# Performance work log

Measured on AMD Instinct MI355X. Metric: run time of the kernel, lower is better.

The kernel has to match this reference:

```python
import jax, jax.numpy as jnp
import numpy as np
import math

B, D_IN, D_MODEL, N_LAYERS, N_HALF, D_OUT = 32, 100, 256, 4, 32, 1
K_ENC = 64               # ConvTranspose2d kernel -> 64x64 feature map from 1x1 latent
L_SEQ = K_ENC * K_ENC    # 4096 flattened spatial sequence for S4D
DT_MIN, DT_MAX = 0.001, 0.1


def setup_inputs() -> dict:
    key = jax.random.key(0)
    ks = jax.random.split(key, 8)
    x = jax.random.normal(ks[0], (B, D_IN, 1, 1), jnp.float32)
    # encoder ConvTranspose2d weight: (in, out, kh, kw)
    enc_w = jax.random.normal(ks[1], (D_IN, D_MODEL, K_ENC, K_ENC), jnp.float32) * 0.02
    # S4D kernel params per layer (stacked over layers)
    log_dt = math.log(DT_MIN) + jax.random.uniform(ks[2], (N_LAYERS, D_MODEL), jnp.float32) * (
        math.log(DT_MAX) - math.log(DT_MIN))
    C = jax.random.normal(ks[3], (N_LAYERS, D_MODEL, N_HALF, 2), jnp.float32)  # complex C as (re, im)
    log_A_real = jnp.log(0.5 * jnp.ones((N_LAYERS, D_MODEL, N_HALF), jnp.float32))
    A_imag = jnp.tile(math.pi * jnp.arange(N_HALF, dtype=jnp.float32), (N_LAYERS, D_MODEL, 1))
    Dskip = jax.random.normal(ks[4], (N_LAYERS, D_MODEL), jnp.float32)
    # output_linear: Conv1d(H, 2H, 1) followed by GLU(dim=-2)
    out_w = jax.random.normal(ks[5], (N_LAYERS, 2 * D_MODEL, D_MODEL), jnp.float32) / math.sqrt(D_MODEL)
    out_b = jnp.zeros((N_LAYERS, 2 * D_MODEL), jnp.float32)
    # decoder: Conv2d(d_model, d_output, 1)
    dec_w = jax.random.normal(ks[6], (D_OUT, D_MODEL), jnp.float32) / math.sqrt(D_MODEL)
    dec_b = jnp.zeros((D_OUT,), jnp.float32)
    return dict(x=x, enc_w=enc_w, log_dt=log_dt, C=C, log_A_real=log_A_real,
                A_imag=A_imag, Dskip=Dskip, out_w=out_w, out_b=out_b,
                dec_w=dec_w, dec_b=dec_b)


def s4d_kernel(log_dt, C, log_A_real, A_imag, L):
    """S4D convolution kernel via Vandermonde: returns (H, L) real kernel."""
    dt = jnp.exp(log_dt)                       # (H,)
    Cc = C[..., 0] + 1j * C[..., 1]            # (H, N)
    A = -jnp.exp(log_A_real) + 1j * A_imag     # (H, N) diagonal state matrix
    dtA = A * dt[:, None]                      # (H, N)
    V = jnp.exp(dtA[:, :, None] * jnp.arange(L, dtype=log_dt.dtype))  # (H, N, L) Vandermonde
    Cc = Cc * (jnp.exp(dtA) - 1.0) / A         # ZOH discretization of C
    return 2.0 * jnp.einsum('hn,hnl->hl', Cc, V).real  # (H, L)


def s4d_layer(u, log_dt, C, log_A_real, A_imag, Dskip, out_w, out_b):
    """u: (B, H, L) -> (B, H, L). FFT convolution + skip + GELU + 1x1 conv + GLU."""
    L = u.shape[-1]
    k = s4d_kernel(log_dt, C, log_A_real, A_imag, L)
    k_f = jnp.fft.rfft(k, n=2 * L)             # (H, L+1)
    u_f = jnp.fft.rfft(u, n=2 * L)             # (B, H, L+1)
    y = jnp.fft.irfft(u_f * k_f, n=2 * L)[..., :L]
    y = y + u * Dskip[:, None]
    y = jax.nn.gelu(y, approximate=False)      # torch nn.GELU (exact erf)
    y = jnp.einsum('oh,bhl->bol', out_w, y) + out_b[:, None]  # Conv1d(H, 2H, 1)
    a, b = jnp.split(y, 2, axis=1)             # GLU along channel dim
    return a * jax.nn.sigmoid(b)


def reference(x, enc_w, log_dt, C, log_A_real, A_imag, Dskip, out_w, out_b, dec_w, dec_b):
    # encoder: ConvTranspose2d(kernel=64, stride=4, bias=False) on a 1x1 input
    # is exactly an outer product of latent with the kernel.
    h = jnp.einsum('bixy,iohw->bohw', x, enc_w)        # (B, D_MODEL, 64, 64)
    Bb, Hc, Hh, Ww = h.shape
    h = h.reshape(Bb, Hc, Hh * Ww)                     # (B, H, L) flattened spatial sequence
    for i in range(N_LAYERS):                          # prenorm=False -> no LayerNorm applied
        z = s4d_layer(h, log_dt[i], C[i], log_A_real[i], A_imag[i],
                      Dskip[i], out_w[i], out_b[i])
        h = z + h                                      # residual
    y = jnp.einsum('oc,bcl->bol', dec_w, h) + dec_b[:, None]  # Conv2d 1x1 decoder
    return y.reshape(Bb, D_OUT, Hh, Ww)
```

## Files before the change

### kernel.cpp

```cpp
#include <hip/hip_runtime.h>
#include <hip/hip_bf16.h>
#include <math.h>

#pragma clang fp contract(off)

#define BB   32
#define DIN  100
#define HH   256
#define NLAY 4
#define NH   32
#define LL   4096
#define LC   128
#define NC   32
#define HL   (HH*LL)
#define BLn  (BB*LL)

typedef __attribute__((ext_vector_type(8))) short s8v;
typedef __attribute__((ext_vector_type(4))) float f4v;

__device__ inline unsigned short f2b(float x) {
    unsigned int u = __float_as_uint(x);
    unsigned int r = (u + 0x7fffu + ((u >> 16) & 1u)) >> 16;
    return (unsigned short)r;
}
__device__ inline float b2f(unsigned short u) {
    return __uint_as_float(((unsigned int)u) << 16);
}

__global__ __launch_bounds__(256) void k_enc(const float* __restrict__ x,
                                             const float* __restrict__ ew,
                                             unsigned short* __restrict__ hb) {
    __shared__ unsigned short xs[BB*128];
    __shared__ unsigned short ot[BB*264];
    int tid = threadIdx.x;
    for (int idx = tid; idx < BB*128; idx += 256) {
        int b = idx >> 7, k = idx & 127;
        float v = (k < DIN) ? x[b*DIN + k] : 0.f;
        int slot = (k >> 3) ^ (b & 7);
        xs[b*128 + slot*8 + (k & 7)] = f2b(v);
    }
    __syncthreads();
    int hl0 = blockIdx.x * 256;
    int h = hl0 >> 12, l0 = hl0 & 4095;
    int w = tid >> 6, l = tid & 63;
    int l16 = l & 15, lk8 = (l >> 4) * 8, e4 = (l >> 4) * 4;
    int col0 = w * 64;
    f4v acc[2][4];
    #pragma unroll
    for (int i = 0; i < 2; i++)
        #pragma unroll
        for (int j = 0; j < 4; j++) acc[i][j] = (f4v){0.f,0.f,0.f,0.f};
    #pragma unroll
    for (int ks = 0; ks < 4; ks++) {
        int kb = ks*32 + lk8;
        int sl0 = kb >> 3;
        s8v a0 = *(const s8v*)&xs[l16*128 + (sl0 ^ (l16 & 7))*8];
        s8v a1 = *(const s8v*)&xs[(16 + l16)*128 + (sl0 ^ (l16 & 7))*8];
        #pragma unroll
        for (int j = 0; j < 4; j++) {
            int hl = hl0 + col0 + j*16 + l16;
            const float* ep = ew + (size_t)kb * HL + hl;
            s8v bf;
            #pragma unroll
            for (int q = 0; q < 8; q++) {
                float ev = (kb + q < DIN) ? ep[(size_t)q * HL] : 0.f;
                bf[q] = (short)f2b(ev);
            }
            acc[0][j] = __builtin_amdgcn_mfma_f32_16x16x32_bf16(a0, bf, acc[0][j], 0, 0, 0);
            acc[1][j] = __builtin_amdgcn_mfma_f32_16x16x32_bf16(a1, bf, acc[1][j], 0, 0, 0);
        }
    }
    #pragma unroll
    for (int i = 0; i < 2; i++)
        #pragma unroll
        for (int j = 0; j < 4; j++) {
            int cl = col0 + j*16 + l16;
            #pragma unroll
            for (int e = 0; e < 4; e++) {
                int b = i*16 + e4 + e;
                ot[b*264 + cl] = f2b(acc[i][j][e]);
            }
        }
    __syncthreads();
    {
        int b = tid >> 3, off = (tid & 7) * 32;
        const unsigned short* src = &ot[b*264 + off];
        unsigned short* dst = &hb[(size_t)h*BLn + (size_t)b*LL + l0 + off];
        #pragma unroll
        for (int q = 0; q < 4; q++)
            *(s8v*)(dst + q*8) = *(const s8v*)(src + q*8);
    }
}

__global__ __launch_bounds__(256) void k_prep1(const float* __restrict__ ldt,
        const float* __restrict__ Cp, const float* __restrict__ lAr,
        const float* __restrict__ Aimp,
        float* __restrict__ pdta, float* __restrict__ pwlc, float* __restrict__ pcd2) {
    int g = blockIdx.x*256 + threadIdx.x;
    int layer = g >> 13, h = (g >> 5) & 255, n = g & 31;
    float dt  = expf(ldt[layer*HH + h]);
    float are = -expf(lAr[(layer*HH + h)*NH + n]);
    float aim = Aimp[(layer*HH + h)*NH + n];
    float dre = are*dt, dimg = aim*dt;
    float er = expf(dre);
    float s, c; sincosf(dimg, &s, &c);
    float wre = er*c, wim = er*s;
    float den = are*are + aim*aim;
    float nre = wre - 1.f, nim = wim;
    float qre = (nre*are + nim*aim)/den;
    float qim = (nim*are - nre*aim)/den;
    float cre = Cp[((layer*HH + h)*NH + n)*2 + 0];
    float cim = Cp[((layer*HH + h)*NH + n)*2 + 1];
    float dcr = cre*qre - cim*qim;
    float dci = cre*qim + cim*qre;
    pcd2[g*2+0] = 2.f*dcr;  pcd2[g*2+1] = 2.f*dci;
    pdta[g*2+0] = dre;      pdta[g*2+1] = dimg;
    float erl = expf(dre*(float)LC);
    float sl, cl; sincosf(dimg*(float)LC, &sl, &cl);
    pwlc[g*2+0] = erl*cl;   pwlc[g*2+1] = erl*sl;
}

__global__ __launch_bounds__(256) void k_bldAll(const float* __restrict__ pdta,
        const float* __restrict__ pcd2, unsigned short* __restrict__ AstB,
        unsigned short* __restrict__ AcvB) {
    __shared__ float dre_s[NH], dim_s[NH], c2r[NH], c2i[NH];
    __shared__ float kkl[LC];
    int bid = blockIdx.x;
    int tid = threadIdx.x;
    int pbase = bid * 64;
    if (tid < NH) {
        dre_s[tid] = pdta[pbase + tid*2];
        dim_s[tid] = pdta[pbase + tid*2 + 1];
        c2r[tid]   = pcd2[pbase + tid*2];
        c2i[tid]   = pcd2[pbase + tid*2 + 1];
    }
    __syncthreads();
    if (tid < LC) {
        float fm = (float)tid;
        float acc = 0.f;
        for (int n = 0; n < NH; n++) {
            float er = expf(dre_s[n]*fm);
            float s, c; sincosf(dim_s[n]*fm, &s, &c);
            acc += c2r[n]*er*c - c2i[n]*er*s;
        }
        kkl[tid] = acc;
    }
    __syncthreads();
    unsigned short* As = AstB + (size_t)bid * 8192;
    for (int idx = tid; idx < 8192; idx += 256) {
        int r = idx >> 7, m = idx & 127, n = r >> 1;
        float e = (float)(127 - m);
        float er = expf(dre_s[n]*e);
        float s, c; sincosf(dim_s[n]*e, &s, &c);
        As[idx] = f2b((r & 1) ? er*s : er*c);
    }
    unsigned short* Ac = AcvB + (size_t)bid * 24576;
    for (int idx = tid; idx < 24576; idx += 256) {
        int j = idx / 192, k = idx - j*192;
        float v;
        if (k < 128) {
            v = (j >= k) ? kkl[j - k] : 0.f;
        } else {
            int n = (k - 128) >> 1;
            float e = (float)(j + 1);
            float er = expf(dre_s[n]*e);
            float s, c; sincosf(dim_s[n]*e, &s, &c);
            v = ((k - 128) & 1) ? (-er*s) : (er*c);
        }
        Ac[idx] = f2b(v);
    }
}

__global__ __launch_bounds__(256) void k_prepW(const float* __restrict__ outw,
                                               unsigned short* __restrict__ Wbf) {
    int t = blockIdx.x*256 + threadIdx.x;
    Wbf[t] = f2b(outw[t]);
}

__global__ __launch_bounds__(256) void k_BG(const unsigned short* __restrict__ AstB,
        const unsigned short* __restrict__ AcvB, const unsigned short* __restrict__ hb,
        const float* __restrict__ pwlc, const float* __restrict__ pcd2,
        const float* __restrict__ DskL, unsigned short* __restrict__ Ybf) {
    __shared__ unsigned short Ul[64*128];
    __shared__ unsigned short Fl[64*64];
    int g = blockIdx.x;
    int h  = (g & 7)*32 + (g >> 7);
    int ct = (g >> 3) & 15;
    int tid = threadIdx.x;
    const unsigned short* ub = hb + (size_t)h*BLn + (size_t)ct*64*LC;
    #pragma unroll
    for (int it = 0; it < 4; it++) {
        int idx = it*256 + tid;
        int col = idx >> 4, slot = idx & 15;
        s8v v = *(const s8v*)(ub + col*LC + slot*8);
        *(s8v*)&Ul[col*128 + (slot ^ (col & 7))*8] = v;
    }
    __syncthreads();
    int w = tid >> 6, l = tid & 63;
    int l16 = l & 15, lk8 = (l >> 4)*8, e4 = (l >> 4)*4, k8q = l >> 4;

    {
        f4v facc[4];
        #pragma unroll
        for (int j = 0; j < 4; j++) facc[j] = (f4v){0.f,0.f,0.f,0.f};
        const unsigned short* Ab = AstB + (size_t)h*8192 + (w*16 + l16)*128;
        #pragma unroll
        for (int ks = 0; ks < 4; ks++) {
            s8v af = *(const s8v*)(Ab + ks*32 + lk8);
            int k8 = ks*4 + k8q;
            #pragma unroll
            for (int j = 0; j < 4; j++) {
                int col = j*16 + l16;
                s8v bf = *(const s8v*)&Ul[col*128 + (k8 ^ (col & 7))*8];
                facc[j] = __builtin_amdgcn_mfma_f32_16x16x32_bf16(af, bf, facc[j], 0, 0, 0);
            }
        }
        #pragma unroll
        for (int j = 0; j < 4; j++) {
            int col = j*16 + l16;
            int idx = (col*64 + w*16 + e4) ^ ((col & 7) << 3);
            *(ushort4*)&Fl[idx] = make_ushort4(f2b(facc[j][0]), f2b(facc[j][1]),
                                               f2b(facc[j][2]), f2b(facc[j][3]));
        }
    }
    __syncthreads();

    if (tid < 64) {
        int n = tid & 31, bl = tid >> 5;
        int hn2 = (h*NH + n)*2;
        float wlr = pwlc[hn2], wli = pwlc[hn2+1];
        float cr  = pcd2[hn2], ci  = pcd2[hn2+1];
        float sr = 0.f, si = 0.f;
        #pragma unroll 4
        for (int c = 0; c < NC; c++) {
            int lcol = bl*32 + c;
            int idx = (lcol*64 + 2*n) ^ ((lcol & 7) << 3);
            ushort2 fv = *(ushort2*)&Fl[idx];
            float fr = b2f(fv.x), fi = b2f(fv.y);
            *(ushort2*)&Fl[idx] = make_ushort2(f2b(cr*sr - ci*si), f2b(cr*si + ci*sr));
            float nsr = fmaf(wlr, sr, fmaf(-wli, si, fr));
            si = fmaf(wlr, si, fmaf(wli, sr, fi));
            sr = nsr;
        }
    }
    __syncthreads();

    float dsk = DskL[h];
    const unsigned short* Cb = AcvB + (size_t)h*24576;
    f4v acc[2][4];
    #pragma unroll
    for (int i = 0; i < 2; i++)
        #pragma unroll
        for (int j = 0; j < 4; j++) acc[i][j] = (f4v){0.f,0.f,0.f,0.f};
    #pragma unroll
    for (int ks = 0; ks < 4; ks++) {
        s8v af0 = *(const s8v*)(Cb + (w*32 + l16)*192 + ks*32 + lk8);
        s8v af1 = *(const s8v*)(Cb + (w*32 + 16 + l16)*192 + ks*32 + lk8);
        int k8 = ks*4 + k8q;
        #pragma unroll
        for (int j = 0; j < 4; j++) {
            int col = j*16 + l16;
            s8v bf = *(const s8v*)&Ul[col*128 + (k8 ^ (col & 7))*8];
            acc[0][j] = __builtin_amdgcn_mfma_f32_16x16x32_bf16(af0, bf, acc[0][j], 0, 0, 0);
            acc[1][j] = __builtin_amdgcn_mfma_f32_16x16x32_bf16(af1, bf, acc[1][j], 0, 0, 0);
        }
    }
    #pragma unroll
    for (int ks = 0; ks < 2; ks++) {
        s8v af0 = *(const s8v*)(Cb + (w*32 + l16)*192 + 128 + ks*32 + lk8);
        s8v af1 = *(const s8v*)(Cb + (w*32 + 16 + l16)*192 + 128 + ks*32 + lk8);
        int kk2 = ks*32 + lk8;
        #pragma unroll
        for (int j = 0; j < 4; j++) {
            int col = j*16 + l16;
            int idx = (col*64 + kk2) ^ ((col & 7) << 3);
            s8v bf = *(const s8v*)&Fl[idx];
            acc[0][j] = __builtin_amdgcn_mfma_f32_16x16x32_bf16(af0, bf, acc[0][j], 0, 0, 0);
            acc[1][j] = __builtin_amdgcn_mfma_f32_16x16x32_bf16(af1, bf, acc[1][j], 0, 0, 0);
        }
    }
    unsigned short* Yb = Ybf + (size_t)h*BLn + (size_t)ct*64*LC;
    #pragma unroll
    for (int i = 0; i < 2; i++) {
        int m0 = w*32 + i*16 + e4;
        int sl = m0 >> 3, off = m0 & 7;
        #pragma unroll
        for (int j = 0; j < 4; j++) {
            int col = j*16 + l16;
            ushort4 u4 = *(const ushort4*)&Ul[col*128 + (sl ^ (col & 7))*8 + off];
            float uu[4] = {b2f(u4.x), b2f(u4.y), b2f(u4.z), b2f(u4.w)};
            unsigned short ov[4];
            #pragma unroll
            for (int e = 0; e < 4; e++) {
                float yv = fmaf(dsk, uu[e], acc[i][j][e]);
                ov[e] = f2b(0.5f*yv*(1.f + erff(yv*0.70710678118f)));
            }
            *(ushort4*)&Yb[col*LC + m0] = make_ushort4(ov[0], ov[1], ov[2], ov[3]);
        }
    }
}

__global__ __launch_bounds__(512) void k_gC2(const unsigned short* __restrict__ Wb,
        const float* __restrict__ outb, const unsigned short* __restrict__ Ybf,
        unsigned short* __restrict__ hb, const float* __restrict__ dw,
        const float* __restrict__ db, float* __restrict__ outp, int doDec) {
    __shared__ __align__(16) unsigned char smem[34048];
    unsigned short* Bl = (unsigned short*)smem;
    float* part = (float*)smem;
    int nt = blockIdx.x;
    int n0 = nt*64;
    int tid = threadIdx.x;

    {
        int jn = (tid & 15) * 4;
        int hq = tid >> 4;
        #pragma unroll
        for (int hb8 = 0; hb8 < 8; hb8++) {
            int h = hb8*32 + hq;
            ushort4 v = *(const ushort4*)&Ybf[(size_t)h*BLn + n0 + jn];
            unsigned short vv[4] = {v.x, v.y, v.z, v.w};
            #pragma unroll
            for (int i = 0; i < 4; i++) {
                int row = jn + i;
                Bl[row*258 + (h ^ ((row & 7) << 3))] = vv[i];
            }
        }
    }
    __syncthreads();

    int w = tid >> 6, l = tid & 63;
    int l16 = l & 15, lk8 = (l >> 4) * 8, e4 = (l >> 4) * 4;
    int ra = w*32 + l16;
    int swz = (l16 & 7) << 3;
    f4v acc[4][4];
    #pragma unroll
    for (int i = 0; i < 4; i++)
        #pragma unroll
        for (int j = 0; j < 4; j++) acc[i][j] = (f4v){0.f,0.f,0.f,0.f};
    const unsigned short* W0 = Wb + ra*HH;
    const unsigned short* W1 = Wb + (ra+16)*HH;
    const unsigned short* W2 = Wb + (ra+256)*HH;
    const unsigned short* W3 = Wb + (ra+272)*HH;
    #pragma unroll
    for (int ks = 0; ks < 8; ks++) {
        int kk = ks*32 + lk8;
        s8v a0 = *(const s8v*)(W0 + kk);
        s8v a1 = *(const s8v*)(W1 + kk);
        s8v a2 = *(const s8v*)(W2 + kk);
        s8v a3 = *(const s8v*)(W3 + kk);
        s8v bfv[4];
        #pragma unroll
        for (int j = 0; j < 4; j++) {
            int row = j*16 + l16;
            bfv[j] = *(const s8v*)&Bl[row*258 + (kk ^ swz)];
        }
        #pragma unroll
        for (int j = 0; j < 4; j++) {
            acc[0][j] = __builtin_amdgcn_mfma_f32_16x16x32_bf16(a0, bfv[j], acc[0][j], 0, 0, 0);
            acc[1][j] = __builtin_amdgcn_mfma_f32_16x16x32_bf16(a1, bfv[j], acc[1][j], 0, 0, 0);
            acc[2][j] = __builtin_amdgcn_mfma_f32_16x16x32_bf16(a2, bfv[j], acc[2][j], 0, 0, 0);
            acc[3][j] = __builtin_amdgcn_mfma_f32_16x16x32_bf16(a3, bfv[j], acc[3][j], 0, 0, 0);
        }
    }

    float pj[4] = {0.f, 0.f, 0.f, 0.f};
    #pragma unroll
    for (int i = 0; i < 2; i++) {
        int ob = w*32 + i*16 + e4;
        #pragma unroll
        for (int e = 0; e < 4; e++) {
            int o = ob + e;
            float ba  = outb[o];
            float bb2 = outb[o + 256];
            float dwo = doDec ? dw[o] : 0.f;
            #pragma unroll
            for (int j = 0; j < 4; j++) {
                float za = acc[i][j][e] + ba;
                float zb = acc[i+2][j][e] + bb2;
                float sig = 1.f/(1.f + expf(-zb));
                unsigned short* hp = &hb[(size_t)o*BLn + n0 + j*16 + l16];
                float hnew = fmaf(za, sig, b2f(*hp));
                if (doDec) {
                    pj[j] = fmaf(dwo, hnew, pj[j]);
                } else {
                    *hp = f2b(hnew);
                }
            }
        }
    }

    if (doDec) {
        __syncthreads();
        int g32 = w*4 + (l >> 4);
        #pragma unroll
        for (int j = 0; j < 4; j++) {
            int nl = j*16 + l16;
            part[nl*33 + g32] = pj[j];
        }
        __syncthreads();
        if (tid < 64) {
            float s = db[0];
            #pragma unroll
            for (int g = 0; g < 32; g++) s += part[tid*33 + g];
            outp[n0 + tid] = s;
        }
    }
}

extern "C" void kernel_launch(void* const* d_in, const int* in_sizes, int n_in,
                              void* d_out, int out_size, void* d_ws, size_t ws_size,
                              hipStream_t stream) {
    (void)in_sizes; (void)n_in; (void)out_size; (void)ws_size;
    const float* x    = (const float*)d_in[0];
    const float* ew   = (const float*)d_in[1];
    const float* ldt  = (const float*)d_in[2];
    const float* Cp   = (const float*)d_in[3];
    const float* lAr  = (const float*)d_in[4];
    const float* Aimp = (const float*)d_in[5];
    const float* Dsk  = (const float*)d_in[6];
    const float* outw = (const float*)d_in[7];
    const float* outb = (const float*)d_in[8];
    const float* dw   = (const float*)d_in[9];
    const float* db   = (const float*)d_in[10];

    float* ws = (float*)d_ws;
    unsigned short* hb  = (unsigned short*)ws;
    unsigned short* Ybf = (unsigned short*)(ws + 16777216UL);
    unsigned short* AstB= (unsigned short*)(ws + 33554432UL);
    unsigned short* AcvB= (unsigned short*)(ws + 37748736UL);
    unsigned short* Wbf = (unsigned short*)(ws + 50331648UL);
    float* pdta = ws + 50593792UL;
    float* pwlc = ws + 50659328UL;
    float* pcd2 = ws + 50724864UL;

    k_prep1<<<128, 256, 0, stream>>>(ldt, Cp, lAr, Aimp, pdta, pwlc, pcd2);
    k_bldAll<<<1024, 256, 0, stream>>>(pdta, pcd2, AstB, AcvB);
    k_prepW<<<2048, 256, 0, stream>>>(outw, Wbf);
    k_enc<<<4096, 256, 0, stream>>>(x, ew, hb);
    for (int layer = 0; layer < NLAY; layer++) {
        k_BG<<<4096, 256, 0, stream>>>(AstB + (size_t)layer*2097152,
                                       AcvB + (size_t)layer*6291456, hb,
                                       pwlc + layer*16384, pcd2 + layer*16384,
                                       Dsk + layer*HH, Ybf);
        k_gC2<<<2048, 512, 0, stream>>>(Wbf + layer*131072, outb + layer*512, Ybf, hb,
                                        dw, db, (float*)d_out, (layer == NLAY-1) ? 1 : 0);
    }
}
```

Before: 990.3 us.

## Fuse per-layer S4D and GLU kernels into a persistent megakernel with flag sync

Replaces the eight per-layer launches of k_BG and k_gC2 with one persistent kernel of 512 blocks. Each block processes several tiles, and the stages are ordered with per-group atomic counters in global memory plus spin waits, so no kernel-boundary barriers are needed. The intent is to cut launch overhead and the tail idle time at each boundary, and to let independent groups move ahead of each other. The risks are a deadlock if not all 512 blocks are co-resident, lower occupancy from the larger shared memory footprint, and spin-wait overhead.

```diff
diff --git a/kernel.cpp b/kernel.cpp
--- a/kernel.cpp
+++ b/kernel.cpp
@@ -29,10 +29,12 @@
 
 __global__ __launch_bounds__(256) void k_enc(const float* __restrict__ x,
                                              const float* __restrict__ ew,
-                                             unsigned short* __restrict__ hb) {
+                                             unsigned short* __restrict__ hb,
+                                             int* __restrict__ flags) {
     __shared__ unsigned short xs[BB*128];
     __shared__ unsigned short ot[BB*264];
     int tid = threadIdx.x;
+    if (blockIdx.x == 0 && tid < 128) flags[tid] = 0;
     for (int idx = tid; idx < BB*128; idx += 256) {
         int b = idx >> 7, k = idx & 127;
         float v = (k < DIN) ? x[b*DIN + k] : 0.f;
@@ -177,16 +179,20 @@
     Wbf[t] = f2b(outw[t]);
 }
 
-__global__ __launch_bounds__(256) void k_BG(const unsigned short* __restrict__ AstB,
-        const unsigned short* __restrict__ AcvB, const unsigned short* __restrict__ hb,
-        const float* __restrict__ pwlc, const float* __restrict__ pcd2,
-        const float* __restrict__ DskL, unsigned short* __restrict__ Ybf) {
-    __shared__ unsigned short Ul[64*128];
-    __shared__ unsigned short Fl[64*64];
-    int g = blockIdx.x;
-    int h  = (g & 7)*32 + (g >> 7);
-    int ct = (g >> 3) & 15;
-    int tid = threadIdx.x;
+__device__ __forceinline__ void waitflag(int* p, int target) {
+    if (threadIdx.x == 0) {
+        while (__hip_atomic_load(p, __ATOMIC_RELAXED, __HIP_MEMORY_SCOPE_AGENT) < target)
+            __builtin_amdgcn_s_sleep(2);
+    }
+    __syncthreads();
+    __threadfence();
+}
+
+__device__ __forceinline__ void bg_tile(unsigned short* Ul, unsigned short* Fl,
+        const unsigned short* AstL, const unsigned short* AcvL,
+        const unsigned short* hb, const float* pwlcL, const float* pcd2L,
+        const float* DskL, unsigned short* Ybf, int h, int ct, int tid) {
+    __syncthreads();
     const unsigned short* ub = hb + (size_t)h*BLn + (size_t)ct*64*LC;
     #pragma unroll
     for (int it = 0; it < 4; it++) {
@@ -203,7 +209,7 @@
         f4v facc[4];
         #pragma unroll
         for (int j = 0; j < 4; j++) facc[j] = (f4v){0.f,0.f,0.f,0.f};
-        const unsigned short* Ab = AstB + (size_t)h*8192 + (w*16 + l16)*128;
+        const unsigned short* Ab = AstL + (size_t)h*8192 + (w*16 + l16)*128;
         #pragma unroll
         for (int ks = 0; ks < 4; ks++) {
             s8v af = *(const s8v*)(Ab + ks*32 + lk8);
@@ -228,8 +234,8 @@
     if (tid < 64) {
         int n = tid & 31, bl = tid >> 5;
         int hn2 = (h*NH + n)*2;
-        float wlr = pwlc[hn2], wli = pwlc[hn2+1];
-        float cr  = pcd2[hn2], ci  = pcd2[hn2+1];
+        float wlr = pwlcL[hn2], wli = pwlcL[hn2+1];
+        float cr  = pcd2L[hn2], ci  = pcd2L[hn2+1];
         float sr = 0.f, si = 0.f;
         #pragma unroll 4
         for (int c = 0; c < NC; c++) {
@@ -246,7 +252,7 @@
     __syncthreads();
 
     float dsk = DskL[h];
-    const unsigned short* Cb = AcvB + (size_t)h*24576;
+    const unsigned short* Cb = AcvL + (size_t)h*24576;
     f4v acc[2][4];
     #pragma unroll
     for (int i = 0; i < 2; i++)
@@ -300,17 +306,14 @@
     }
 }
 
-__global__ __launch_bounds__(512) void k_gC2(const unsigned short* __restrict__ Wb,
-        const float* __restrict__ outb, const unsigned short* __restrict__ Ybf,
-        unsigned short* __restrict__ hb, const float* __restrict__ dw,
-        const float* __restrict__ db, float* __restrict__ outp, int doDec) {
-    __shared__ __align__(16) unsigned char smem[34048];
+__device__ __forceinline__ void gc2_tile(unsigned char* smem,
+        const unsigned short* WbL, const float* outbL,
+        const unsigned short* Ybf, unsigned short* hb, const float* dw,
+        const float* db, float* outp, int nt, int doDec, int tid) {
     unsigned short* Bl = (unsigned short*)smem;
     float* part = (float*)smem;
-    int nt = blockIdx.x;
     int n0 = nt*64;
-    int tid = threadIdx.x;
-
+    __syncthreads();
     {
         int jn = (tid & 15) * 4;
         int hq = tid >> 4;
@@ -337,10 +340,10 @@
     for (int i = 0; i < 4; i++)
         #pragma unroll
         for (int j = 0; j < 4; j++) acc[i][j] = (f4v){0.f,0.f,0.f,0.f};
-    const unsigned short* W0 = Wb + ra*HH;
-    const unsigned short* W1 = Wb + (ra+16)*HH;
-    const unsigned short* W2 = Wb + (ra+256)*HH;
-    const unsigned short* W3 = Wb + (ra+272)*HH;
+    const unsigned short* W0 = WbL + ra*HH;
+    const unsigned short* W1 = WbL + (ra+16)*HH;
+    const unsigned short* W2 = WbL + (ra+256)*HH;
+    const unsigned short* W3 = WbL + (ra+272)*HH;
     #pragma unroll
     for (int ks = 0; ks < 8; ks++) {
         int kk = ks*32 + lk8;
@@ -370,8 +373,8 @@
         #pragma unroll
         for (int e = 0; e < 4; e++) {
             int o = ob + e;
-            float ba  = outb[o];
-            float bb2 = outb[o + 256];
+            float ba  = outbL[o];
+            float bb2 = outbL[o + 256];
             float dwo = doDec ? dw[o] : 0.f;
             #pragma unroll
             for (int j = 0; j < 4; j++) {
@@ -403,6 +406,58 @@
             #pragma unroll
             for (int g = 0; g < 32; g++) s += part[tid*33 + g];
             outp[n0 + tid] = s;
+        }
+    }
+}
+
+__global__ __launch_bounds__(512, 4) void k_mega(
+        const unsigned short* __restrict__ AstB, const unsigned short* __restrict__ AcvB,
+        unsigned short* __restrict__ hb, unsigned short* __restrict__ Ybf,
+        const float* __restrict__ pwlc, const float* __restrict__ pcd2,
+        const float* __restrict__ Dsk, const unsigned short* __restrict__ Wbf,
+        const float* __restrict__ outb, const float* __restrict__ dw,
+        const float* __restrict__ db, float* __restrict__ outp,
+        int* __restrict__ flags) {
+    __shared__ __align__(16) unsigned char smem[49664];
+    int tid = threadIdx.x;
+    int g = blockIdx.x;
+    int s = tid >> 8;
+    int tid256 = tid & 255;
+    int grp = g >> 5;
+    unsigned short* Ul = (unsigned short*)(smem + s*24576);
+    unsigned short* Fl = (unsigned short*)(smem + s*24576 + 16384);
+    int* cnt1 = flags;
+    int* cnt2 = flags + 64;
+
+    for (int L = 0; L < NLAY; L++) {
+        if (L) waitflag(&cnt2[(L-1)*16 + grp], 128);
+        const unsigned short* AstL = AstB + (size_t)L*2097152;
+        const unsigned short* AcvL = AcvB + (size_t)L*6291456;
+        const float* pwlcL = pwlc + L*16384;
+        const float* pcd2L = pcd2 + L*16384;
+        const float* DskL  = Dsk + L*HH;
+        #pragma unroll 1
+        for (int i = 0; i < 4; i++) {
+            int T = g*8 + s*4 + i;
+            bg_tile(Ul, Fl, AstL, AcvL, hb, pwlcL, pcd2L, DskL, Ybf,
+                    T & 255, T >> 8, tid256);
+        }
+        __threadfence();
+        __syncthreads();
+        if (tid == 0) atomicAdd(&cnt1[L*16 + grp], 8);
+        waitflag(&cnt1[L*16 + grp], 256);
+
+        const unsigned short* WbL  = Wbf + L*131072;
+        const float* outbL = outb + L*512;
+        int doDec = (L == NLAY-1) ? 1 : 0;
+        #pragma unroll 1
+        for (int j = 0; j < 4; j++) {
+            gc2_tile(smem, WbL, outbL, Ybf, hb, dw, db, outp, g*4 + j, doDec, tid);
+        }
+        if (L < NLAY-1) {
+            __threadfence();
+            __syncthreads();
+            if (tid == 0) atomicAdd(&cnt2[L*16 + grp], 4);
         }
     }
 }
@@ -432,17 +487,12 @@
     float* pdta = ws + 50593792UL;
     float* pwlc = ws + 50659328UL;
     float* pcd2 = ws + 50724864UL;
+    int*   flg  = (int*)(ws + 50790400UL);
 
     k_prep1<<<128, 256, 0, stream>>>(ldt, Cp, lAr, Aimp, pdta, pwlc, pcd2);
     k_bldAll<<<1024, 256, 0, stream>>>(pdta, pcd2, AstB, AcvB);
     k_prepW<<<2048, 256, 0, stream>>>(outw, Wbf);
-    k_enc<<<4096, 256, 0, stream>>>(x, ew, hb);
-    for (int layer = 0; layer < NLAY; layer++) {
-        k_BG<<<4096, 256, 0, stream>>>(AstB + (size_t)layer*2097152,
-                                       AcvB + (size_t)layer*6291456, hb,
-                                       pwlc + layer*16384, pcd2 + layer*16384,
-                                       Dsk + layer*HH, Ybf);
-        k_gC2<<<2048, 512, 0, stream>>>(Wbf + layer*131072, outb + layer*512, Ybf, hb,
-                                        dw, db, (float*)d_out, (layer == NLAY-1) ? 1 : 0);
-    }
-}
+    k_enc<<<4096, 256, 0, stream>>>(x, ew, hb, flg);
+    k_mega<<<512, 512, 0, stream>>>(AstB, AcvB, hb, Ybf, pwlc, pcd2, Dsk,
+                                    Wbf, outb, dw, db, (float*)d_out, flg);
+}
```

Measured after the change: 3.918 ms. 296% more time.
